# Optimization experiments

Measured on AMD Instinct MI355X. Metric: run time of the kernel, lower is better.

The kernel has to match this reference:

```python
import jax, jax.numpy as jnp
from jax import lax
import numpy as np

B, F, C, H, W = 2, 2, 3, 256, 512
D = 32
INV_DEPTH_MAX, INV_DEPTH_MIN = 1.0 / 3.0, 1.0 / 80.0
ALPHA = 10.0
PATCH = 3
BORDER = PATCH // 2 + 1  # border_radius = 2
CW = jnp.array([5 / 32, 16 / 32, 11 / 32], dtype=jnp.float32)
C1, C2 = 0.01 ** 2, 0.03 ** 2


def _avg3(x):
    # reflection-pad 1 + 3x3 avg pool, stride 1 (monodepth2 SSIM)
    xp = jnp.pad(x, ((0, 0), (0, 0), (1, 1), (1, 1)), mode='reflect')
    return lax.reduce_window(xp, 0.0, lax.add, (1, 1, 3, 3), (1, 1, 1, 1), 'VALID') / 9.0


def ssim(x, y):
    mu_x, mu_y = _avg3(x), _avg3(y)
    sigma_x = _avg3(x * x) - mu_x ** 2
    sigma_y = _avg3(y * y) - mu_y ** 2
    sigma_xy = _avg3(x * y) - mu_x * mu_y
    n = (2 * mu_x * mu_y + C1) * (2 * sigma_xy + C2)
    d = (mu_x ** 2 + mu_y ** 2 + C1) * (sigma_x + sigma_y + C2)
    return jnp.clip((1.0 - n / d) / 2.0, 0.0, 1.0)


def _boxsum3(x):
    # 3x3 zero-padded box sum over the last two dims of [F,D,H,W] (== conv3d with 1x3x3 ones)
    return lax.reduce_window(x, 0.0, lax.add, (1, 1, 3, 3), (1, 1, 1, 1),
                             ((0, 0), (0, 0), (1, 1), (1, 1)))


def grid_sample(img, grid):
    # bilinear, zeros padding, align_corners=False; img [N,Ch,H,W], grid [N,H,W,2] in [-1,1]
    N, Ch, Hh, Ww = img.shape
    x = (grid[..., 0] + 1.0) * (Ww * 0.5) - 0.5
    y = (grid[..., 1] + 1.0) * (Hh * 0.5) - 0.5
    x0 = jnp.floor(x)
    y0 = jnp.floor(y)

    def gather(im, xi, yi):
        valid = (xi >= 0) & (xi <= Ww - 1) & (yi >= 0) & (yi <= Hh - 1)
        xc = jnp.clip(xi, 0, Ww - 1).astype(jnp.int32)
        yc = jnp.clip(yi, 0, Hh - 1).astype(jnp.int32)
        return im[:, yc, xc] * valid[None]

    def sample_one(im, xx, yy, xx0, yy0):
        xx1, yy1 = xx0 + 1, yy0 + 1
        wa = (xx1 - xx) * (yy1 - yy)
        wb = (xx1 - xx) * (yy - yy0)
        wc = (xx - xx0) * (yy1 - yy)
        wd = (xx - xx0) * (yy - yy0)
        return (gather(im, xx0, yy0) * wa + gather(im, xx0, yy1) * wb +
                gather(im, xx1, yy0) * wc + gather(im, xx1, yy1) * wd)

    return jax.vmap(sample_one)(img, x, y, x0, y0)


def setup_inputs() -> dict:
    key = jax.random.key(0)
    k1, k2 = jax.random.split(key)
    keyframe = jax.random.uniform(k1, (B, C, H, W), jnp.float32, -0.5, 0.5)
    frames = jax.random.uniform(k2, (F, B, C, H, W), jnp.float32, -0.5, 0.5)
    K = np.eye(4, dtype=np.float32)
    K[0, 0] = 0.58 * W; K[1, 1] = 1.92 * H; K[0, 2] = 0.5 * W; K[1, 2] = 0.5 * H
    keyframe_intrinsics = jnp.broadcast_to(jnp.asarray(K), (B, 4, 4))
    intrinsics = jnp.broadcast_to(jnp.asarray(K), (F, B, 4, 4))
    keyframe_pose = jnp.broadcast_to(jnp.eye(4, dtype=jnp.float32), (B, 4, 4))
    poses_np = np.zeros((F, B, 4, 4), dtype=np.float32)
    for f in range(F):
        for b in range(B):
            ang = 0.02 * (f + 1) * (1.0 if b % 2 == 0 else -1.0)
            c, s = np.cos(ang), np.sin(ang)
            Tm = np.eye(4, dtype=np.float32)
            Tm[:3, :3] = np.array([[c, 0, s], [0, 1, 0], [-s, 0, c]], dtype=np.float32)
            Tm[0, 3] = 0.3 * (f + 1)
            Tm[2, 3] = 0.5 * (f + 1)
            poses_np[f, b] = Tm
    return {'keyframe': keyframe, 'frames': frames,
            'keyframe_intrinsics': keyframe_intrinsics, 'intrinsics': intrinsics,
            'keyframe_pose': keyframe_pose, 'poses': jnp.asarray(poses_np)}


def reference(keyframe, frames, keyframe_intrinsics, intrinsics, keyframe_pose, poses):
    dt = keyframe.dtype
    depths = (1.0 / jnp.linspace(INV_DEPTH_MAX, INV_DEPTH_MIN, D)).astype(dt)  # [D]
    xs, ys = jnp.meshgrid(jnp.arange(W, dtype=dt), jnp.arange(H, dtype=dt))    # 'xy'
    coord = jnp.stack([xs.ravel(), ys.ravel(), jnp.ones(H * W, dt)], 0)        # [3,HW]
    border_mask = jnp.zeros((1, H, W), dt).at[:, BORDER:H - BORDER, BORDER:W - BORDER].set(1.0)

    def per_batch(kf, kK, kpose, frs, Ks, ps):
        inv_k = jnp.linalg.inv(kK)
        cam = inv_k[:3, :3] @ coord                      # [3,HW]
        cam_pts = depths[:, None, None] * cam[None]      # [D,3,HW]
        cam_pts4 = jnp.concatenate([cam_pts, jnp.ones((D, 1, H * W), dt)], 1)

        def warp(fr, Kf, pf):
            T = jnp.linalg.inv(pf) @ kpose
            P = (Kf @ T)[:3]                             # [3,4]
            cp = jnp.einsum('ij,djn->din', P, cam_pts4)  # [D,3,HW]
            pix = cp[:, :2] / (cp[:, 2:3] + 1e-7)
            pix = pix.reshape(D, 2, H, W).transpose(0, 2, 3, 1)
            gx = pix[..., 0] / (W - 1)
            gy = pix[..., 1] / (H - 1)
            grid = jnp.clip((jnp.stack([gx, gy], -1) - 0.5) * 2.0, -2.0, 2.0)
            wimg = grid_sample(jnp.broadcast_to(fr, (D, C, H, W)), grid)        # [D,C,H,W]
            wm = grid_sample(jnp.broadcast_to(border_mask[None], (D, 1, H, W)), grid)
            wmask = border_mask * jnp.all(wm != 0, axis=0)                      # [1,H,W]
            return wimg, wmask

        wimgs, wmasks = jax.vmap(warp)(frs, Ks, ps)      # [F,D,C,H,W], [F,1,H,W]
        diff = ssim(wimgs.reshape(F * D, C, H, W) + 0.5,
                    jnp.broadcast_to(kf + 0.5, (F * D, C, H, W))).reshape(F, D, C, H, W)
        # conv3d SAD: channel-weighted sum then 3x3 zero-pad box sum / patch^2
        sad = _boxsum3(jnp.einsum('fdchw,c->fdhw', diff, CW.astype(dt))) / (PATCH * PATCH)
        sfcv = (1.0 - 2.0 * sad) * wmasks                # [F,D,H,W]
        sum_item = jnp.exp(-ALPHA * (sad - jnp.min(sad, 1, keepdims=True)) ** 2)
        weight = (1.0 - (jnp.sum(sum_item, 1, keepdims=True) - 1.0) / (D - 1)) * wmasks  # [F,1,H,W]
        cv = jnp.sum(sad * weight, 0)                    # [D,H,W]
        ws = jnp.sum(weight, 0)[0]                       # [H,W]
        wz = ws == 0
        cv = jnp.where(wz[None], 0.0, 1.0 - 2.0 * cv / jnp.where(wz, 1.0, ws)[None])
        return cv, sfcv

    cost_volume, sfcvs = jax.vmap(per_batch, in_axes=(0, 0, 0, 1, 1, 1))(
        keyframe, keyframe_intrinsics, keyframe_pose, frames, intrinsics, poses)
    # cost_volume [B,D,H,W]; single_frame_cvs as [F,B,D,H,W]
    return cost_volume, jnp.moveaxis(sfcvs, 1, 0)
```

## Files before the change

kernel.cpp:

```cpp
#include <hip/hip_runtime.h>

#define BB 2
#define FF 2
#define CC 3
#define HH 256
#define WW 512
#define DD 32
#define HW (HH*WW)
#define CV_SIZE (BB*DD*HW)

#define SH 16
#define NSTRIP (HH/SH)
#define NTHR 128
#define INV9 (1.0f/9.0f)
#define C1f 1e-4f
#define C2f 9e-4f

__device__ __forceinline__ int refl(int i, int n) { return i < 0 ? -i : (i >= n ? 2*n-2-i : i); }

__device__ void inv4(const float* m, float* out) {
  float a[4][8];
  for (int i = 0; i < 4; ++i)
    for (int j = 0; j < 4; ++j) { a[i][j] = m[i*4+j]; a[i][j+4] = (i==j) ? 1.f : 0.f; }
  for (int col = 0; col < 4; ++col) {
    int piv = col; float best = fabsf(a[col][col]);
    for (int r = col+1; r < 4; ++r) { float v = fabsf(a[r][col]); if (v > best) { best = v; piv = r; } }
    if (piv != col) for (int j = 0; j < 8; ++j) { float t = a[col][j]; a[col][j] = a[piv][j]; a[piv][j] = t; }
    float invd = 1.0f / a[col][col];
    for (int j = 0; j < 8; ++j) a[col][j] *= invd;
    for (int r = 0; r < 4; ++r) {
      if (r == col) continue;
      float f = a[r][col];
      for (int j = 0; j < 8; ++j) a[r][j] -= f * a[col][j];
    }
  }
  for (int i = 0; i < 4; ++i) for (int j = 0; j < 4; ++j) out[i*4+j] = a[i][j+4];
}

__global__ void setup_kernel(const float* __restrict__ kK, const float* __restrict__ Ks,
                             const float* __restrict__ kpose, const float* __restrict__ poses,
                             float* __restrict__ P, float* __restrict__ IK, float* __restrict__ M) {
  __shared__ float sIK[BB][9];
  __shared__ float sP[FF*BB][12];
  int t = threadIdx.x;
  if (t < BB) {
    float inv[16]; inv4(kK + t*16, inv);
    float* o = IK + t*9;
    float v0=inv[0], v1=inv[1], v2=inv[2], v3=inv[4], v4=inv[5], v5=inv[6], v6=inv[8], v7=inv[9], v8=inv[10];
    o[0]=v0;o[1]=v1;o[2]=v2;o[3]=v3;o[4]=v4;o[5]=v5;o[6]=v6;o[7]=v7;o[8]=v8;
    sIK[t][0]=v0;sIK[t][1]=v1;sIK[t][2]=v2;sIK[t][3]=v3;sIK[t][4]=v4;sIK[t][5]=v5;sIK[t][6]=v6;sIK[t][7]=v7;sIK[t][8]=v8;
  }
  if (t >= 32 && t < 32 + FF*BB) {
    int i = t - 32;
    int b = i % BB;
    float ip[16]; inv4(poses + i*16, ip);
    float T[16];
    for (int r = 0; r < 4; ++r)
      for (int c = 0; c < 4; ++c) {
        float s = 0.f;
        for (int k = 0; k < 4; ++k) s += ip[r*4+k] * kpose[b*16 + k*4 + c];
        T[r*4+c] = s;
      }
    for (int r = 0; r < 3; ++r)
      for (int c = 0; c < 4; ++c) {
        float s = 0.f;
        for (int k = 0; k < 4; ++k) s += Ks[i*16 + r*4 + k] * T[k*4 + c];
        P[i*12 + r*4 + c] = s;
        sP[i][r*4+c] = s;
      }
  }
  __syncthreads();
  if (t < FF*BB*DD) {
    int fb = t / DD, d = t % DD, b = fb % BB;
    const float invd0 = 1.0f/3.0f;
    const float step  = (0.0125f - (1.0f/3.0f)) / 31.0f;
    float depth = 1.0f / (invd0 + step * (float)d);
    for (int i = 0; i < 3; ++i)
      for (int j = 0; j < 3; ++j) {
        float s = sP[fb][i*4+0]*sIK[b][0*3+j] + sP[fb][i*4+1]*sIK[b][1*3+j] + sP[fb][i*4+2]*sIK[b][2*3+j];
        float mv = depth*s + ((j==2) ? sP[fb][i*4+3] : 0.f);
        M[t*12 + i*3 + j] = mv;
      }
  }
}

__global__ void kfstats_kernel(const float* __restrict__ kf, float* __restrict__ muy,
                               float* __restrict__ sigy) {
  int idx = blockIdx.x*blockDim.x + threadIdx.x;
  if (idx >= BB*CC*HW) return;
  int w = idx % WW, h = (idx/WW) % HH;
  int bc = idx / HW;
  const float* ys = kf + bc*HW;
  float s = 0.f, s2 = 0.f;
  #pragma unroll
  for (int dy = -1; dy <= 1; ++dy) {
    int rh = refl(h+dy, HH);
    #pragma unroll
    for (int dx = -1; dx <= 1; ++dx) {
      int rw = refl(w+dx, WW);
      float yv = ys[rh*WW+rw] + 0.5f;
      s += yv; s2 += yv*yv;
    }
  }
  float mu = s / 9.0f;
  muy[idx] = mu;
  sigy[idx] = s2/9.0f - mu*mu;
}

#define SAMPLE(slot, hrarg) do { \
  int hr_ = (hrarg); \
  float fh_ = (float)hr_; \
  float b0_ = fmaf(m01, fh_, m02); \
  float b1_ = fmaf(m11, fh_, m12); \
  float b2_ = fmaf(m21, fh_, m22); \
  _Pragma("unroll") \
  for (int c_ = 0; c_ < CC; ++c_) { \
    const float4 yv_ = *(const float4*)(kfb + c_*HW + hr_*WW + w0); \
    yr[c_][slot][0] = yv_.x + 0.5f; yr[c_][slot][1] = yv_.y + 0.5f; \
    yr[c_][slot][2] = yv_.z + 0.5f; yr[c_][slot][3] = yv_.w + 0.5f; \
  } \
  _Pragma("unroll") \
  for (int k_ = 0; k_ < 4; ++k_) { \
    float fw_ = (float)(w0 + k_); \
    float cp0_ = fmaf(m00, fw_, b0_); \
    float cp1_ = fmaf(m10, fw_, b1_); \
    float cp2_ = fmaf(m20, fw_, b2_); \
    float den_ = cp2_ + 1e-7f; \
    float rd_ = __builtin_amdgcn_rcpf(den_); \
    float px_ = cp0_*rd_, py_ = cp1_*rd_; \
    float gx_ = fminf(fmaxf((px_*(1.0f/511.0f) - 0.5f)*2.0f, -2.0f), 2.0f); \
    float gy_ = fminf(fmaxf((py_*(1.0f/255.0f) - 0.5f)*2.0f, -2.0f), 2.0f); \
    float x_ = (gx_ + 1.0f)*((float)WW*0.5f) - 0.5f; \
    float y_ = (gy_ + 1.0f)*((float)HH*0.5f) - 0.5f; \
    float x0f_ = floorf(x_), y0f_ = floorf(y_); \
    float x1f_ = x0f_ + 1.f, y1f_ = y0f_ + 1.f; \
    float wa_ = (x1f_-x_)*(y1f_-y_); \
    float wb_ = (x1f_-x_)*(y_-y0f_); \
    float wc_ = (x_-x0f_)*(y1f_-y_); \
    float wd_ = (x_-x0f_)*(y_-y0f_); \
    bool vx0_ = (x0f_ >= 0.f) && (x0f_ <= (float)(WW-1)); \
    bool vx1_ = (x1f_ >= 0.f) && (x1f_ <= (float)(WW-1)); \
    bool vy0_ = (y0f_ >= 0.f) && (y0f_ <= (float)(HH-1)); \
    bool vy1_ = (y1f_ >= 0.f) && (y1f_ <= (float)(HH-1)); \
    int xi0_ = (int)fminf(fmaxf(x0f_, 0.f), (float)(WW-1)); \
    int xi1_ = (int)fminf(fmaxf(x1f_, 0.f), (float)(WW-1)); \
    int yi0_ = (int)fminf(fmaxf(y0f_, 0.f), (float)(HH-1)); \
    int yi1_ = (int)fminf(fmaxf(y1f_, 0.f), (float)(HH-1)); \
    int i00_ = yi0_*WW + xi0_, i01_ = yi1_*WW + xi0_; \
    int i10_ = yi0_*WW + xi1_, i11_ = yi1_*WW + xi1_; \
    _Pragma("unroll") \
    for (int c_ = 0; c_ < CC; ++c_) { \
      const float* im_ = frame + c_*HW; \
      float va_ = (vx0_ && vy0_) ? im_[i00_] : 0.f; \
      float vb2_ = (vx0_ && vy1_) ? im_[i01_] : 0.f; \
      float vc2_ = (vx1_ && vy0_) ? im_[i10_] : 0.f; \
      float vd2_ = (vx1_ && vy1_) ? im_[i11_] : 0.f; \
      xr[c_][slot][k_] = fmaf(va_, wa_, fmaf(vb2_, wb_, fmaf(vc2_, wc_, vd2_*wd_))) + 0.5f; \
    } \
  } \
} while (0)

#define HSUM(arr, v, o) do { \
  float L_ = sb[pb][arr][1][tm]; \
  float R_ = sb[pb][arr][0][tp]; \
  if (t == 0) L_ = (v)[1]; \
  if (t == NTHR-1) R_ = (v)[2]; \
  float p01_ = (v)[0] + (v)[1]; \
  float p12_ = (v)[1] + (v)[2]; \
  float p23_ = (v)[2] + (v)[3]; \
  (o)[0] = L_ + p01_; (o)[1] = p01_ + (v)[2]; \
  (o)[2] = p12_ + (v)[3]; (o)[3] = p23_ + R_; \
} while (0)

__global__ __launch_bounds__(NTHR) void wss2_kernel(
    const float* __restrict__ frames, const float* __restrict__ keyframe,
    const float* __restrict__ M, const float* __restrict__ muy, const float* __restrict__ sigy,
    float* __restrict__ sadout) {
  __shared__ float sb[2][10][2][NTHR];

  int bid = blockIdx.x;
  int strip = bid & (NSTRIP-1);
  int d  = (bid >> 4) & (DD-1);
  int fb = bid >> 9;
  int b = fb % BB;
  int h0 = strip * SH;
  int t = threadIdx.x;
  int w0 = t*4;
  int tm = (t > 0) ? t-1 : 0;
  int tp = (t < NTHR-1) ? t+1 : NTHR-1;

  const float* Mp = M + (fb*DD + d)*12;
  float m00=Mp[0], m01=Mp[1], m02=Mp[2];
  float m10=Mp[3], m11=Mp[4], m12=Mp[5];
  float m20=Mp[6], m21=Mp[7], m22=Mp[8];
  const float* frame = frames + (size_t)fb*CC*HW;
  const float* kfb   = keyframe + (size_t)b*CC*HW;
  const float* muyb  = muy + (size_t)b*CC*HW;
  const float* sigyb = sigy + (size_t)b*CC*HW;
  float* sadp = sadout + (size_t)(fb*DD + d)*HW;

  float xr[CC][3][4], yr[CC][3][4], df[3][4];
  #pragma unroll
  for (int k = 0; k < 4; ++k) { df[0][k]=0.f; df[1][k]=0.f; df[2][k]=0.f; }

  SAMPLE(0, refl(h0-2, HH));
  SAMPLE(1, refl(h0-1, HH));

  for (int r = h0-1; r <= h0+SH+1; ++r) {
    int pb = r & 1;
    SAMPLE(2, refl(r+1, HH));
    float vs[CC][3][4];
    #pragma unroll
    for (int c = 0; c < CC; ++c) {
      #pragma unroll
      for (int k = 0; k < 4; ++k) {
        float x0 = xr[c][0][k], x1 = xr[c][1][k], x2 = xr[c][2][k];
        float y0 = yr[c][0][k], y1 = yr[c][1][k], y2 = yr[c][2][k];
        vs[c][0][k] = (x0 + x1) + x2;
        vs[c][1][k] = fmaf(x2, x2, fmaf(x1, x1, x0*x0));
        vs[c][2][k] = fmaf(x2, y2, fmaf(x1, y1, x0*y0));
      }
      sb[pb][c*3+0][0][t] = vs[c][0][0]; sb[pb][c*3+0][1][t] = vs[c][0][3];
      sb[pb][c*3+1][0][t] = vs[c][1][0]; sb[pb][c*3+1][1][t] = vs[c][1][3];
      sb[pb][c*3+2][0][t] = vs[c][2][0]; sb[pb][c*3+2][1][t] = vs[c][2][3];
    }
    float vb[4];
    #pragma unroll
    for (int k = 0; k < 4; ++k) vb[k] = (df[0][k] + df[1][k]) + df[2][k];
    sb[pb][9][0][t] = vb[0]; sb[pb][9][1][t] = vb[3];
    __syncthreads();

    #pragma unroll
    for (int k = 0; k < 4; ++k) { df[0][k] = df[1][k]; df[1][k] = df[2][k]; }
    bool rowvalid = (r >= 0) && (r < HH);
    float nd[4] = {0.f, 0.f, 0.f, 0.f};
    if (rowvalid) {
      float accv[4] = {0.f, 0.f, 0.f, 0.f};
      #pragma unroll
      for (int c = 0; c < CC; ++c) {
        float hx[4], hxx[4], hxy[4];
        HSUM(c*3+0, vs[c][0], hx);
        HSUM(c*3+1, vs[c][1], hxx);
        HSUM(c*3+2, vs[c][2], hxy);
        const float4 mu4 = *(const float4*)(muyb + c*HW + r*WW + w0);
        const float4 sg4 = *(const float4*)(sigyb + c*HW + r*WW + w0);
        float muv[4] = {mu4.x, mu4.y, mu4.z, mu4.w};
        float sgv[4] = {sg4.x, sg4.y, sg4.z, sg4.w};
        float cwc = (c==0) ? (5.f/32.f) : ((c==1) ? (16.f/32.f) : (11.f/32.f));
        #pragma unroll
        for (int k = 0; k < 4; ++k) {
          float mux = hx[k]*INV9;
          float sigx = fmaf(-mux, mux, hxx[k]*INV9);
          float sigxy = fmaf(-mux, muv[k], hxy[k]*INV9);
          float nn  = (2.f*mux*muv[k] + C1f) * (2.f*sigxy + C2f);
          float ddn = fmaf(mux, mux, fmaf(muv[k], muv[k], C1f)) * ((sigx + sgv[k]) + C2f);
          float v = (1.f - nn*__builtin_amdgcn_rcpf(ddn))*0.5f;
          v = fminf(fmaxf(v, 0.f), 1.f);
          accv[k] = fmaf(cwc, v, accv[k]);
        }
      }
      nd[0]=accv[0]; nd[1]=accv[1]; nd[2]=accv[2]; nd[3]=accv[3];
    }
    df[2][0]=nd[0]; df[2][1]=nd[1]; df[2][2]=nd[2]; df[2][3]=nd[3];

    int s = r - 2;
    if (s >= h0 && s < h0 + SH) {
      float Lb = (t == 0)      ? 0.f : sb[pb][9][1][tm];
      float Rb = (t == NTHR-1) ? 0.f : sb[pb][9][0][tp];
      float p01 = vb[0]+vb[1], p12 = vb[1]+vb[2], p23 = vb[2]+vb[3];
      float4 o;
      o.x = (Lb + p01)*INV9;
      o.y = (p01 + vb[2])*INV9;
      o.z = (p12 + vb[3])*INV9;
      o.w = (p23 + Rb)*INV9;
      *(float4*)(sadp + (size_t)s*WW + w0) = o;
    }
    #pragma unroll
    for (int c = 0; c < CC; ++c)
      #pragma unroll
      for (int k = 0; k < 4; ++k) {
        xr[c][0][k]=xr[c][1][k]; xr[c][1][k]=xr[c][2][k];
        yr[c][0][k]=yr[c][1][k]; yr[c][1][k]=yr[c][2][k];
      }
  }
}

struct Proj { float x, y; };

__device__ __forceinline__ Proj project(const float* __restrict__ Pm,
                                        float camx, float camy, float camz, int d) {
  const float invd0 = 1.0f/3.0f;
  const float step  = (0.0125f - (1.0f/3.0f)) / 31.0f;
  float depth = 1.0f / (invd0 + step * (float)d);
  float X = depth*camx, Y = depth*camy, Z = depth*camz;
  float cp0 = Pm[0]*X + Pm[1]*Y + Pm[2]*Z  + Pm[3];
  float cp1 = Pm[4]*X + Pm[5]*Y + Pm[6]*Z  + Pm[7];
  float cp2 = Pm[8]*X + Pm[9]*Y + Pm[10]*Z + Pm[11];
  float den = cp2 + 1e-7f;
  float px = cp0 / den;
  float py = cp1 / den;
  float gx = px / (float)(WW-1);
  float gy = py / (float)(HH-1);
  gx = fminf(fmaxf((gx - 0.5f)*2.0f, -2.0f), 2.0f);
  gy = fminf(fmaxf((gy - 0.5f)*2.0f, -2.0f), 2.0f);
  Proj pr;
  pr.x = (gx + 1.0f) * ((float)WW*0.5f) - 0.5f;
  pr.y = (gy + 1.0f) * ((float)HH*0.5f) - 0.5f;
  return pr;
}

__device__ __forceinline__ float borderVal(float xif, float yif) {
  if (!((xif >= 0.f) && (xif <= (float)(WW-1)) && (yif >= 0.f) && (yif <= (float)(HH-1)))) return 0.f;
  int xi = (int)xif, yi = (int)yif;
  return (xi >= 2 && xi < WW-2 && yi >= 2 && yi < HH-2) ? 1.f : 0.f;
}

__global__ __launch_bounds__(256) void final_kernel(
    const float* __restrict__ P, const float* __restrict__ IK,
    float* __restrict__ out) {
  int idx = blockIdx.x*blockDim.x + threadIdx.x;
  if (idx >= BB*HW) return;
  int p = idx % HW;
  int b = idx / HW;
  int w = p % WW, h = p / WW;
  float* sadbase = out + CV_SIZE;
  bool inb = (w >= 2 && w < WW-2 && h >= 2 && h < HH-2);

  float fw = (float)w, fh = (float)h;
  const float* ik = IK + b*9;
  float camx = ik[0]*fw + ik[1]*fh + ik[2];
  float camy = ik[3]*fw + ik[4]*fh + ik[5];
  float camz = ik[6]*fw + ik[7]*fh + ik[8];

  float cv[DD];
  #pragma unroll
  for (int d = 0; d < DD; ++d) cv[d] = 0.f;
  float wsum = 0.f;

  for (int f = 0; f < FF; ++f) {
    int fb = f*BB + b;
    const float* Pm = P + fb*12;
    bool ok = true;
    for (int d = 0; d < DD; ++d) {
      Proj pr = project(Pm, camx, camy, camz, d);
      float x = pr.x, y = pr.y;
      float x0f = floorf(x), y0f = floorf(y);
      float x1f = x0f+1.f, y1f = y0f+1.f;
      float wa = (x1f-x)*(y1f-y);
      float wb = (x1f-x)*(y-y0f);
      float wc = (x-x0f)*(y1f-y);
      float wd = (x-x0f)*(y-y0f);
      float m = borderVal(x0f,y0f)*wa + borderVal(x0f,y1f)*wb +
                borderVal(x1f,y0f)*wc + borderVal(x1f,y1f)*wd;
      ok = ok && (m != 0.f);
    }
    float wmask = (inb && ok) ? 1.f : 0.f;

    float* sfb = sadbase + (size_t)fb*DD*HW + p;
    float sv[DD];
    float mn = 3.0e38f;
    #pragma unroll
    for (int d = 0; d < DD; ++d) { sv[d] = sfb[(size_t)d*HW]; mn = fminf(mn, sv[d]); }
    float s = 0.f;
    #pragma unroll
    for (int d = 0; d < DD; ++d) { float tt = sv[d] - mn; s += expf(-10.f*tt*tt); }
    float wt = (1.f - (s - 1.f)/31.f) * wmask;
    wsum += wt;
    #pragma unroll
    for (int d = 0; d < DD; ++d) {
      cv[d] += sv[d]*wt;
      sfb[(size_t)d*HW] = (1.f - 2.f*sv[d]) * wmask;
    }
  }
  #pragma unroll
  for (int d = 0; d < DD; ++d)
    out[((size_t)b*DD + d)*HW + p] = (wsum == 0.f) ? 0.f : 1.f - 2.f*cv[d]/wsum;
}

extern "C" void kernel_launch(void* const* d_in, const int* in_sizes, int n_in,
                              void* d_out, int out_size, void* d_ws, size_t ws_size,
                              hipStream_t stream) {
  const float* keyframe = (const float*)d_in[0];
  const float* frames   = (const float*)d_in[1];
  const float* kK       = (const float*)d_in[2];
  const float* Ks       = (const float*)d_in[3];
  const float* kpose    = (const float*)d_in[4];
  const float* poses    = (const float*)d_in[5];
  float* out = (float*)d_out;

  float* wsP   = (float*)d_ws;
  float* wsIK  = wsP + 64;
  float* wsM   = wsIK + 64;
  float* wsMuy = (float*)d_ws + 2048;
  float* wsSigy= wsMuy + BB*CC*HW;

  setup_kernel<<<1, 128, 0, stream>>>(kK, Ks, kpose, poses, wsP, wsIK, wsM);
  kfstats_kernel<<<(BB*CC*HW + 255)/256, 256, 0, stream>>>(keyframe, wsMuy, wsSigy);
  wss2_kernel<<<FF*BB*DD*NSTRIP, NTHR, 0, stream>>>(frames, keyframe, wsM, wsMuy, wsSigy, out + CV_SIZE);
  final_kernel<<<(BB*HW + 255)/256, 256, 0, stream>>>(wsP, wsIK, out);
}
```

Measured before the change: 300.4 us.

## Split SSIM rows into single-wavefront halves using shuffles and halo recompute

The fused warp+SSIM+SAD kernel now runs each row strip as two independent 64-thread blocks, one wavefront each covering half the image width. Shared memory and per-row __syncthreads give way to wavefront shuffles for neighbour sums. Each lane also recomputes one halo column so the half-width blocks need no data exchange. This adds redundant sampling and SSIM work for the halo columns, and the final kernel switches expf to the faster __expf intrinsic.

```diff
diff --git a/kernel.cpp b/kernel.cpp
--- a/kernel.cpp
+++ b/kernel.cpp
@@ -11,7 +11,7 @@
 
 #define SH 16
 #define NSTRIP (HH/SH)
-#define NTHR 128
+#define HALFW 256
 #define INV9 (1.0f/9.0f)
 #define C1f 1e-4f
 #define C2f 9e-4f
@@ -107,87 +107,73 @@
   sigy[idx] = s2/9.0f - mu*mu;
 }
 
-#define SAMPLE(slot, hrarg) do { \
-  int hr_ = (hrarg); \
-  float fh_ = (float)hr_; \
-  float b0_ = fmaf(m01, fh_, m02); \
-  float b1_ = fmaf(m11, fh_, m12); \
-  float b2_ = fmaf(m21, fh_, m22); \
-  _Pragma("unroll") \
-  for (int c_ = 0; c_ < CC; ++c_) { \
-    const float4 yv_ = *(const float4*)(kfb + c_*HW + hr_*WW + w0); \
-    yr[c_][slot][0] = yv_.x + 0.5f; yr[c_][slot][1] = yv_.y + 0.5f; \
-    yr[c_][slot][2] = yv_.z + 0.5f; yr[c_][slot][3] = yv_.w + 0.5f; \
-  } \
-  _Pragma("unroll") \
-  for (int k_ = 0; k_ < 4; ++k_) { \
-    float fw_ = (float)(w0 + k_); \
-    float cp0_ = fmaf(m00, fw_, b0_); \
-    float cp1_ = fmaf(m10, fw_, b1_); \
-    float cp2_ = fmaf(m20, fw_, b2_); \
-    float den_ = cp2_ + 1e-7f; \
-    float rd_ = __builtin_amdgcn_rcpf(den_); \
-    float px_ = cp0_*rd_, py_ = cp1_*rd_; \
-    float gx_ = fminf(fmaxf((px_*(1.0f/511.0f) - 0.5f)*2.0f, -2.0f), 2.0f); \
-    float gy_ = fminf(fmaxf((py_*(1.0f/255.0f) - 0.5f)*2.0f, -2.0f), 2.0f); \
-    float x_ = (gx_ + 1.0f)*((float)WW*0.5f) - 0.5f; \
-    float y_ = (gy_ + 1.0f)*((float)HH*0.5f) - 0.5f; \
-    float x0f_ = floorf(x_), y0f_ = floorf(y_); \
-    float x1f_ = x0f_ + 1.f, y1f_ = y0f_ + 1.f; \
-    float wa_ = (x1f_-x_)*(y1f_-y_); \
-    float wb_ = (x1f_-x_)*(y_-y0f_); \
-    float wc_ = (x_-x0f_)*(y1f_-y_); \
-    float wd_ = (x_-x0f_)*(y_-y0f_); \
-    bool vx0_ = (x0f_ >= 0.f) && (x0f_ <= (float)(WW-1)); \
-    bool vx1_ = (x1f_ >= 0.f) && (x1f_ <= (float)(WW-1)); \
-    bool vy0_ = (y0f_ >= 0.f) && (y0f_ <= (float)(HH-1)); \
-    bool vy1_ = (y1f_ >= 0.f) && (y1f_ <= (float)(HH-1)); \
-    int xi0_ = (int)fminf(fmaxf(x0f_, 0.f), (float)(WW-1)); \
-    int xi1_ = (int)fminf(fmaxf(x1f_, 0.f), (float)(WW-1)); \
-    int yi0_ = (int)fminf(fmaxf(y0f_, 0.f), (float)(HH-1)); \
-    int yi1_ = (int)fminf(fmaxf(y1f_, 0.f), (float)(HH-1)); \
-    int i00_ = yi0_*WW + xi0_, i01_ = yi1_*WW + xi0_; \
-    int i10_ = yi0_*WW + xi1_, i11_ = yi1_*WW + xi1_; \
-    _Pragma("unroll") \
-    for (int c_ = 0; c_ < CC; ++c_) { \
-      const float* im_ = frame + c_*HW; \
-      float va_ = (vx0_ && vy0_) ? im_[i00_] : 0.f; \
-      float vb2_ = (vx0_ && vy1_) ? im_[i01_] : 0.f; \
-      float vc2_ = (vx1_ && vy0_) ? im_[i10_] : 0.f; \
-      float vd2_ = (vx1_ && vy1_) ? im_[i11_] : 0.f; \
-      xr[c_][slot][k_] = fmaf(va_, wa_, fmaf(vb2_, wb_, fmaf(vc2_, wc_, vd2_*wd_))) + 0.5f; \
-    } \
-  } \
-} while (0)
-
-#define HSUM(arr, v, o) do { \
-  float L_ = sb[pb][arr][1][tm]; \
-  float R_ = sb[pb][arr][0][tp]; \
-  if (t == 0) L_ = (v)[1]; \
-  if (t == NTHR-1) R_ = (v)[2]; \
-  float p01_ = (v)[0] + (v)[1]; \
-  float p12_ = (v)[1] + (v)[2]; \
-  float p23_ = (v)[2] + (v)[3]; \
-  (o)[0] = L_ + p01_; (o)[1] = p01_ + (v)[2]; \
-  (o)[2] = p12_ + (v)[3]; (o)[3] = p23_ + R_; \
-} while (0)
-
-__global__ __launch_bounds__(NTHR) void wss2_kernel(
+struct F3 { float v[CC]; };
+
+__device__ __forceinline__ F3 sample_col(const float* __restrict__ frame,
+    float m00, float m10, float m20, float b0, float b1, float b2, float fw) {
+  float cp0 = fmaf(m00, fw, b0);
+  float cp1 = fmaf(m10, fw, b1);
+  float cp2 = fmaf(m20, fw, b2);
+  float den = cp2 + 1e-7f;
+  float rd = __builtin_amdgcn_rcpf(den);
+  float px = cp0*rd, py = cp1*rd;
+  float gx = fminf(fmaxf((px*(1.0f/511.0f) - 0.5f)*2.0f, -2.0f), 2.0f);
+  float gy = fminf(fmaxf((py*(1.0f/255.0f) - 0.5f)*2.0f, -2.0f), 2.0f);
+  float x = (gx + 1.0f)*((float)WW*0.5f) - 0.5f;
+  float y = (gy + 1.0f)*((float)HH*0.5f) - 0.5f;
+  float x0f = floorf(x), y0f = floorf(y);
+  float x1f = x0f + 1.f, y1f = y0f + 1.f;
+  float wa = (x1f-x)*(y1f-y);
+  float wb = (x1f-x)*(y-y0f);
+  float wc = (x-x0f)*(y1f-y);
+  float wd = (x-x0f)*(y-y0f);
+  bool vx0 = (x0f >= 0.f) && (x0f <= (float)(WW-1));
+  bool vx1 = (x1f >= 0.f) && (x1f <= (float)(WW-1));
+  bool vy0 = (y0f >= 0.f) && (y0f <= (float)(HH-1));
+  bool vy1 = (y1f >= 0.f) && (y1f <= (float)(HH-1));
+  int xi0 = (int)fminf(fmaxf(x0f, 0.f), (float)(WW-1));
+  int xi1 = (int)fminf(fmaxf(x1f, 0.f), (float)(WW-1));
+  int yi0 = (int)fminf(fmaxf(y0f, 0.f), (float)(HH-1));
+  int yi1 = (int)fminf(fmaxf(y1f, 0.f), (float)(HH-1));
+  int i00 = yi0*WW + xi0, i01 = yi1*WW + xi0;
+  int i10 = yi0*WW + xi1, i11 = yi1*WW + xi1;
+  F3 o;
+  #pragma unroll
+  for (int c = 0; c < CC; ++c) {
+    const float* im = frame + c*HW;
+    float va = (vx0 && vy0) ? im[i00] : 0.f;
+    float vb2 = (vx0 && vy1) ? im[i01] : 0.f;
+    float vc2 = (vx1 && vy0) ? im[i10] : 0.f;
+    float vd2 = (vx1 && vy1) ? im[i11] : 0.f;
+    o.v[c] = fmaf(va, wa, fmaf(vb2, wb, fmaf(vc2, wc, vd2*wd))) + 0.5f;
+  }
+  return o;
+}
+
+__device__ __forceinline__ float ssim_term(float hx, float hxx, float hxy, float mu_y, float sg_y) {
+  float mux = hx*INV9;
+  float sigx = fmaf(-mux, mux, hxx*INV9);
+  float sigxy = fmaf(-mux, mu_y, hxy*INV9);
+  float nn  = (2.f*mux*mu_y + C1f) * (2.f*sigxy + C2f);
+  float ddn = fmaf(mux, mux, fmaf(mu_y, mu_y, C1f)) * ((sigx + sg_y) + C2f);
+  float v = (1.f - nn*__builtin_amdgcn_rcpf(ddn))*0.5f;
+  return fminf(fmaxf(v, 0.f), 1.f);
+}
+
+__global__ __launch_bounds__(64) void wss3_kernel(
     const float* __restrict__ frames, const float* __restrict__ keyframe,
     const float* __restrict__ M, const float* __restrict__ muy, const float* __restrict__ sigy,
     float* __restrict__ sadout) {
-  __shared__ float sb[2][10][2][NTHR];
-
   int bid = blockIdx.x;
-  int strip = bid & (NSTRIP-1);
-  int d  = (bid >> 4) & (DD-1);
-  int fb = bid >> 9;
+  int half  = bid & 1;
+  int strip = (bid >> 1) & (NSTRIP-1);
+  int d     = (bid >> 5) & (DD-1);
+  int fb    = bid >> 10;
   int b = fb % BB;
   int h0 = strip * SH;
-  int t = threadIdx.x;
-  int w0 = t*4;
-  int tm = (t > 0) ? t-1 : 0;
-  int tp = (t < NTHR-1) ? t+1 : NTHR-1;
+  int l = threadIdx.x;
+  int w0 = half*HALFW + l*4;
+  int hc = half ? (255 - l) : (319 - l);
 
   const float* Mp = M + (fb*DD + d)*12;
   float m00=Mp[0], m01=Mp[1], m02=Mp[2];
@@ -199,17 +185,62 @@
   const float* sigyb = sigy + (size_t)b*CC*HW;
   float* sadp = sadout + (size_t)(fb*DD + d)*HW;
 
-  float xr[CC][3][4], yr[CC][3][4], df[3][4];
+  float xr[CC][3][4], yr[CC][3][4];
+  float hxr[CC][3], hyr[CC][3];
+  float df[3][4], hdf[3];
   #pragma unroll
   for (int k = 0; k < 4; ++k) { df[0][k]=0.f; df[1][k]=0.f; df[2][k]=0.f; }
-
-  SAMPLE(0, refl(h0-2, HH));
-  SAMPLE(1, refl(h0-1, HH));
-
-  for (int r = h0-1; r <= h0+SH+1; ++r) {
-    int pb = r & 1;
-    SAMPLE(2, refl(r+1, HH));
-    float vs[CC][3][4];
+  hdf[0]=0.f; hdf[1]=0.f; hdf[2]=0.f;
+
+  float fwk[4], fhc = (float)hc;
+  #pragma unroll
+  for (int k = 0; k < 4; ++k) fwk[k] = (float)(w0 + k);
+
+#define SAMPLE_ROW(slot, hrarg) do { \
+    int hr_ = (hrarg); \
+    float fh_ = (float)hr_; \
+    float b0_ = fmaf(m01, fh_, m02); \
+    float b1_ = fmaf(m11, fh_, m12); \
+    float b2_ = fmaf(m21, fh_, m22); \
+    _Pragma("unroll") \
+    for (int c_ = 0; c_ < CC; ++c_) { \
+      const float4 yv_ = *(const float4*)(kfb + c_*HW + hr_*WW + w0); \
+      yr[c_][slot][0] = yv_.x + 0.5f; yr[c_][slot][1] = yv_.y + 0.5f; \
+      yr[c_][slot][2] = yv_.z + 0.5f; yr[c_][slot][3] = yv_.w + 0.5f; \
+      hyr[c_][slot] = kfb[c_*HW + hr_*WW + hc] + 0.5f; \
+    } \
+    _Pragma("unroll") \
+    for (int k_ = 0; k_ < 4; ++k_) { \
+      F3 s_ = sample_col(frame, m00, m10, m20, b0_, b1_, b2_, fwk[k_]); \
+      xr[0][slot][k_] = s_.v[0]; xr[1][slot][k_] = s_.v[1]; xr[2][slot][k_] = s_.v[2]; \
+    } \
+    { F3 s_ = sample_col(frame, m00, m10, m20, b0_, b1_, b2_, fhc); \
+      hxr[0][slot] = s_.v[0]; hxr[1][slot] = s_.v[1]; hxr[2][slot] = s_.v[2]; } \
+  } while (0)
+
+  SAMPLE_ROW(0, refl(h0-2, HH));
+  SAMPLE_ROW(1, refl(h0-1, HH));
+
+#define STORE_SAD(srow, VB, HVB) do { \
+    float Lb_ = __shfl_up((VB)[3], 1); \
+    float Rb_ = __shfl_down((VB)[0], 1); \
+    if (l == 0)  Lb_ = half ? (HVB) : 0.f; \
+    if (l == 63) Rb_ = half ? 0.f : (HVB); \
+    float p01_ = (VB)[0]+(VB)[1], p12_ = (VB)[1]+(VB)[2], p23_ = (VB)[2]+(VB)[3]; \
+    float4 o_; \
+    o_.x = (Lb_ + p01_)*INV9; \
+    o_.y = (p01_ + (VB)[2])*INV9; \
+    o_.z = (p12_ + (VB)[3])*INV9; \
+    o_.w = (p23_ + Rb_)*INV9; \
+    *(float4*)(sadp + (size_t)(srow)*WW + w0) = o_; \
+  } while (0)
+
+  #pragma unroll 3
+  for (int i = 0; i < SH+2; ++i) {
+    int r = h0 - 1 + i;
+    SAMPLE_ROW(2, refl(r+1, HH));
+
+    float vs[CC][3][4], hvs[CC][3];
     #pragma unroll
     for (int c = 0; c < CC; ++c) {
       #pragma unroll
@@ -220,68 +251,84 @@
         vs[c][1][k] = fmaf(x2, x2, fmaf(x1, x1, x0*x0));
         vs[c][2][k] = fmaf(x2, y2, fmaf(x1, y1, x0*y0));
       }
-      sb[pb][c*3+0][0][t] = vs[c][0][0]; sb[pb][c*3+0][1][t] = vs[c][0][3];
-      sb[pb][c*3+1][0][t] = vs[c][1][0]; sb[pb][c*3+1][1][t] = vs[c][1][3];
-      sb[pb][c*3+2][0][t] = vs[c][2][0]; sb[pb][c*3+2][1][t] = vs[c][2][3];
-    }
-    float vb[4];
-    #pragma unroll
-    for (int k = 0; k < 4; ++k) vb[k] = (df[0][k] + df[1][k]) + df[2][k];
-    sb[pb][9][0][t] = vb[0]; sb[pb][9][1][t] = vb[3];
-    __syncthreads();
+      float hx0 = hxr[c][0], hx1 = hxr[c][1], hx2 = hxr[c][2];
+      float hy0 = hyr[c][0], hy1 = hyr[c][1], hy2 = hyr[c][2];
+      hvs[c][0] = (hx0 + hx1) + hx2;
+      hvs[c][1] = fmaf(hx2, hx2, fmaf(hx1, hx1, hx0*hx0));
+      hvs[c][2] = fmaf(hx2, hy2, fmaf(hx1, hy1, hx0*hy0));
+    }
+
+    int s = r - 2;
+    if (s >= h0) {
+      float vb[4];
+      #pragma unroll
+      for (int k = 0; k < 4; ++k) vb[k] = (df[0][k] + df[1][k]) + df[2][k];
+      float hvb = (hdf[0] + hdf[1]) + hdf[2];
+      STORE_SAD(s, vb, hvb);
+    }
 
     #pragma unroll
     for (int k = 0; k < 4; ++k) { df[0][k] = df[1][k]; df[1][k] = df[2][k]; }
-    bool rowvalid = (r >= 0) && (r < HH);
-    float nd[4] = {0.f, 0.f, 0.f, 0.f};
-    if (rowvalid) {
-      float accv[4] = {0.f, 0.f, 0.f, 0.f};
+    hdf[0] = hdf[1]; hdf[1] = hdf[2];
+    float nd[4] = {0.f,0.f,0.f,0.f};
+    float hnd = 0.f;
+    if (r >= 0 && r < HH) {
+      float accv[4] = {0.f,0.f,0.f,0.f};
+      float hacc = 0.f;
       #pragma unroll
       for (int c = 0; c < CC; ++c) {
-        float hx[4], hxx[4], hxy[4];
-        HSUM(c*3+0, vs[c][0], hx);
-        HSUM(c*3+1, vs[c][1], hxx);
-        HSUM(c*3+2, vs[c][2], hxy);
+        float hsum[3][4], hh[3];
+        #pragma unroll
+        for (int a = 0; a < 3; ++a) {
+          const float* v = vs[c][a];
+          float hv = hvs[c][a];
+          float L = __shfl_up(v[3], 1);
+          float R = __shfl_down(v[0], 1);
+          if (l == 0)  L = half ? hv : v[1];
+          if (l == 63) R = half ? v[2] : hv;
+          float p01 = v[0]+v[1], p12 = v[1]+v[2], p23 = v[2]+v[3];
+          hsum[a][0] = L + p01; hsum[a][1] = p01 + v[2];
+          hsum[a][2] = p12 + v[3]; hsum[a][3] = p23 + R;
+          float hL = half ? __shfl_down(hv, 1) : v[3];
+          float hR = half ? v[0] : __shfl_up(hv, 1);
+          hh[a] = (hL + hv) + hR;
+        }
         const float4 mu4 = *(const float4*)(muyb + c*HW + r*WW + w0);
         const float4 sg4 = *(const float4*)(sigyb + c*HW + r*WW + w0);
+        float hmu = muyb[c*HW + r*WW + hc];
+        float hsg = sigyb[c*HW + r*WW + hc];
         float muv[4] = {mu4.x, mu4.y, mu4.z, mu4.w};
         float sgv[4] = {sg4.x, sg4.y, sg4.z, sg4.w};
         float cwc = (c==0) ? (5.f/32.f) : ((c==1) ? (16.f/32.f) : (11.f/32.f));
         #pragma unroll
-        for (int k = 0; k < 4; ++k) {
-          float mux = hx[k]*INV9;
-          float sigx = fmaf(-mux, mux, hxx[k]*INV9);
-          float sigxy = fmaf(-mux, muv[k], hxy[k]*INV9);
-          float nn  = (2.f*mux*muv[k] + C1f) * (2.f*sigxy + C2f);
-          float ddn = fmaf(mux, mux, fmaf(muv[k], muv[k], C1f)) * ((sigx + sgv[k]) + C2f);
-          float v = (1.f - nn*__builtin_amdgcn_rcpf(ddn))*0.5f;
-          v = fminf(fmaxf(v, 0.f), 1.f);
-          accv[k] = fmaf(cwc, v, accv[k]);
-        }
+        for (int k = 0; k < 4; ++k)
+          accv[k] = fmaf(cwc, ssim_term(hsum[0][k], hsum[1][k], hsum[2][k], muv[k], sgv[k]), accv[k]);
+        hacc = fmaf(cwc, ssim_term(hh[0], hh[1], hh[2], hmu, hsg), hacc);
       }
       nd[0]=accv[0]; nd[1]=accv[1]; nd[2]=accv[2]; nd[3]=accv[3];
+      hnd = hacc;
     }
     df[2][0]=nd[0]; df[2][1]=nd[1]; df[2][2]=nd[2]; df[2][3]=nd[3];
-
-    int s = r - 2;
-    if (s >= h0 && s < h0 + SH) {
-      float Lb = (t == 0)      ? 0.f : sb[pb][9][1][tm];
-      float Rb = (t == NTHR-1) ? 0.f : sb[pb][9][0][tp];
-      float p01 = vb[0]+vb[1], p12 = vb[1]+vb[2], p23 = vb[2]+vb[3];
-      float4 o;
-      o.x = (Lb + p01)*INV9;
-      o.y = (p01 + vb[2])*INV9;
-      o.z = (p12 + vb[3])*INV9;
-      o.w = (p23 + Rb)*INV9;
-      *(float4*)(sadp + (size_t)s*WW + w0) = o;
-    }
-    #pragma unroll
-    for (int c = 0; c < CC; ++c)
+    hdf[2] = hnd;
+
+    #pragma unroll
+    for (int c = 0; c < CC; ++c) {
       #pragma unroll
       for (int k = 0; k < 4; ++k) {
         xr[c][0][k]=xr[c][1][k]; xr[c][1][k]=xr[c][2][k];
         yr[c][0][k]=yr[c][1][k]; yr[c][1][k]=yr[c][2][k];
       }
+      hxr[c][0]=hxr[c][1]; hxr[c][1]=hxr[c][2];
+      hyr[c][0]=hyr[c][1]; hyr[c][1]=hyr[c][2];
+    }
+  }
+
+  {
+    float vb[4];
+    #pragma unroll
+    for (int k = 0; k < 4; ++k) vb[k] = (df[0][k] + df[1][k]) + df[2][k];
+    float hvb = (hdf[0] + hdf[1]) + hdf[2];
+    STORE_SAD(h0+SH-1, vb, hvb);
   }
 }
 
@@ -363,7 +410,7 @@
     for (int d = 0; d < DD; ++d) { sv[d] = sfb[(size_t)d*HW]; mn = fminf(mn, sv[d]); }
     float s = 0.f;
     #pragma unroll
-    for (int d = 0; d < DD; ++d) { float tt = sv[d] - mn; s += expf(-10.f*tt*tt); }
+    for (int d = 0; d < DD; ++d) { float tt = sv[d] - mn; s += __expf(-10.f*tt*tt); }
     float wt = (1.f - (s - 1.f)/31.f) * wmask;
     wsum += wt;
     #pragma unroll
@@ -396,6 +443,6 @@
 
   setup_kernel<<<1, 128, 0, stream>>>(kK, Ks, kpose, poses, wsP, wsIK, wsM);
   kfstats_kernel<<<(BB*CC*HW + 255)/256, 256, 0, stream>>>(keyframe, wsMuy, wsSigy);
-  wss2_kernel<<<FF*BB*DD*NSTRIP, NTHR, 0, stream>>>(frames, keyframe, wsM, wsMuy, wsSigy, out + CV_SIZE);
+  wss3_kernel<<<FF*BB*DD*NSTRIP*2, 64, 0, stream>>>(frames, keyframe, wsM, wsMuy, wsSigy, out + CV_SIZE);
   final_kernel<<<(BB*HW + 255)/256, 256, 0, stream>>>(wsP, wsIK, out);
 }
```

Result: slower. 436.1 us (+45.2%).
